# Optimization experiments

Measured on AMD Instinct MI355X. Metric: run time of the kernel, lower is better.

Reference implementation:

```python
import jax, jax.numpy as jnp
import numpy as np

MAXHD, MAXV, MINA, MAXA, DT = 100.0, 40.0, -6.0, 4.0, 0.1
NVEH, NT, IN_DIM, UNITS = 4096, 1024, 12, 20


def setup_inputs() -> dict:
    key = jax.random.key(0)
    ks = jax.random.split(key, 12)
    leadfol_inputs = jax.random.normal(ks[0], (NVEH, NT, IN_DIM), dtype=jnp.float32)
    init_state = jax.random.normal(ks[1], (NVEH, 2), dtype=jnp.float32)
    hidden_states = jnp.zeros((2, NVEH, UNITS), dtype=jnp.float32)
    s = 0.1
    return {
        "leadfol_inputs": leadfol_inputs,
        "init_state": init_state,
        "hidden_states": hidden_states,
        "kernel": s * jax.random.normal(ks[2], (IN_DIM, 4 * UNITS), dtype=jnp.float32),
        "rkernel": s * jax.random.normal(ks[3], (UNITS, 4 * UNITS), dtype=jnp.float32),
        "bias": jnp.zeros((4 * UNITS,), dtype=jnp.float32),
        "W2": s * jax.random.normal(ks[4], (UNITS, 10), dtype=jnp.float32),
        "b2": jnp.zeros((10,), dtype=jnp.float32),
        "Wlc": s * jax.random.normal(ks[5], (10, 3), dtype=jnp.float32),
        "blc": jnp.zeros((3,), dtype=jnp.float32),
        "W1": s * jax.random.normal(ks[6], (10, 1), dtype=jnp.float32),
        "b1": jnp.zeros((1,), dtype=jnp.float32),
    }


def reference(leadfol_inputs, init_state, hidden_states, kernel, rkernel, bias,
              W2, b2, Wlc, blc, W1, b1):
    # time-major for scan: (nt, nveh, 12)
    xs = jnp.transpose(leadfol_inputs, (1, 0, 2))
    pos0, spd0 = init_state[:, 0], init_state[:, 1]
    h0, c0 = hidden_states[0], hidden_states[1]

    def step(carry, x_t):
        pos, spd, h, c = carry
        lead_hd = (x_t[:, :3] - pos[:, None]) / MAXHD
        fol_hd = (pos[:, None] - x_t[:, 3:6]) / MAXHD
        spds = x_t[:, 6:] / MAXV
        inp = jnp.concatenate([lead_hd, fol_hd, spds], axis=1)  # (nveh, 12)
        inp = jnp.where(jnp.isnan(inp), jnp.ones_like(inp), inp)
        # Keras LSTMCell (inference, no dropout): gate order i, f, g, o
        z = inp @ kernel + h @ rkernel + bias
        i_g, f_g, g_g, o_g = jnp.split(z, 4, axis=1)
        c_new = jax.nn.sigmoid(f_g) * c + jax.nn.sigmoid(i_g) * jnp.tanh(g_g)
        h_new = jax.nn.sigmoid(o_g) * jnp.tanh(c_new)
        x2 = jax.nn.relu(h_new @ W2 + b2)          # (nveh, 10)
        lc = x2 @ Wlc + blc                          # (nveh, 3)
        acc_raw = (x2 @ W1 + b1)[:, 0]               # (nveh,)
        acc = (MAXA - MINA) * acc_raw + MINA
        pos_new = pos + DT * spd
        spd_new = spd + DT * acc
        return (pos_new, spd_new, h_new, c_new), (pos_new, lc)

    (pos_f, spd_f, h_f, c_f), (traj, lc_all) = jax.lax.scan(step, (pos0, spd0, h0, c0), xs)
    pred_traj = jnp.transpose(traj, (1, 0))            # (nveh, nt)
    pred_lc_action = jnp.transpose(lc_all, (1, 0, 2))  # (nveh, nt, 3)
    return pred_traj, pred_lc_action, spd_f, (h_f, c_f)
```

## Files before the change

kernel.cpp:

```cpp
#include <hip/hip_runtime.h>
#include <cstdint>

#define NVEH  4096
#define NT    1024
#define INW   12
#define UNITS 20

typedef float f32x2 __attribute__((ext_vector_type(2)));

#define PIN(v)  asm volatile("" : "+v"(v))

#define PKFMA_LO(acc, w, s2) \
    asm("v_pk_fma_f32 %0, %1, %2, %0 op_sel:[0,0,0] op_sel_hi:[1,0,1]" \
        : "+v"(acc) : "v"(w), "v"(s2))
#define PKFMA_HI(acc, w, s2) \
    asm("v_pk_fma_f32 %0, %1, %2, %0 op_sel:[0,1,0] op_sel_hi:[1,1,1]" \
        : "+v"(acc) : "v"(w), "v"(s2))
#define PKMUL_LO(dst, w, s2) \
    asm("v_pk_mul_f32 %0, %1, %2 op_sel:[0,0] op_sel_hi:[1,0]" \
        : "=v"(dst) : "v"(w), "v"(s2))
#define PKMUL_HI(dst, w, s2) \
    asm("v_pk_mul_f32 %0, %1, %2 op_sel:[0,1] op_sel_hi:[1,1]" \
        : "=v"(dst) : "v"(w), "v"(s2))

__device__ __forceinline__ float fexp2(float x) { return __builtin_amdgcn_exp2f(x); }
__device__ __forceinline__ float frcp(float x)  { return __builtin_amdgcn_rcpf(x); }

__device__ __forceinline__ void gload_lds16(const float* g, float* l) {
    __builtin_amdgcn_global_load_lds(
        (const __attribute__((address_space(1))) unsigned int*)g,
        (__attribute__((address_space(3))) unsigned int*)l,
        16, 0, 0);
}

__global__ __attribute__((amdgpu_waves_per_eu(2, 2))) __launch_bounds__(64)
void rnncf_kernel(const float* __restrict__ x,
                  const float* __restrict__ init_state,
                  const float* __restrict__ hs,
                  const float* __restrict__ K,
                  const float* __restrict__ R,
                  const float* __restrict__ bias,
                  const float* __restrict__ W2,
                  const float* __restrict__ b2,
                  const float* __restrict__ Wlc,
                  const float* __restrict__ blc,
                  const float* __restrict__ W1,
                  const float* __restrict__ b1,
                  float* __restrict__ out)
{
    const int lane = threadIdx.x;
    const int grp  = lane / 20;
    const int sub  = lane % 20;
    const int veh  = blockIdx.x * 3 + grp;
    const bool active = (grp < 3) && (veh < NVEH);
    const int vs = active ? veh : 0;

    __shared__ __align__(16) float x_lds[8][4][12];
    __shared__ __align__(16) float h_lds[4][20];
    __shared__ __align__(16) float x2_lds[4][12];

    const float s01l = -1.4426950408889634f;
    const float s01h = -1.4426950408889634f;
    const float s23l =  2.8853900817779268f;
    const float s23h = -1.4426950408889634f;
    f32x2 K01[12], K23[12], R01[20], R23[20], bz01, bz23;
    bz01[0] = s01l * bias[sub];      bz01[1] = s01h * bias[20 + sub];
    bz23[0] = s23l * bias[40 + sub]; bz23[1] = s23h * bias[60 + sub];
#pragma unroll
    for (int k = 0; k < 12; ++k) {
        K01[k][0] = s01l * K[k * 80 + sub];      K01[k][1] = s01h * K[k * 80 + 20 + sub];
        K23[k][0] = s23l * K[k * 80 + 40 + sub]; K23[k][1] = s23h * K[k * 80 + 60 + sub];
    }
#pragma unroll
    for (int k = 0; k < 20; ++k) {
        R01[k][0] = s01l * R[k * 80 + sub];      R01[k][1] = s01h * R[k * 80 + 20 + sub];
        R23[k][0] = s23l * R[k * 80 + 40 + sub]; R23[k][1] = s23h * R[k * 80 + 60 + sub];
    }
    const int mh = (sub < 10) ? sub : 9;
    f32x2 W2p[10];
#pragma unroll
    for (int u = 0; u < 10; ++u) {
        W2p[u][0] = W2[(2 * u) * 10 + mh];
        W2p[u][1] = W2[(2 * u + 1) * 10 + mh];
    }
    float b2s = b2[mh];
    const int jl = (sub < 3) ? sub : 0;
    f32x2 Wlcp[5];
#pragma unroll
    for (int m = 0; m < 5; ++m) {
        Wlcp[m][0] = Wlc[(2 * m) * 3 + jl];
        Wlcp[m][1] = Wlc[(2 * m + 1) * 3 + jl];
    }
    float blcs = blc[jl];
    PIN(bz01); PIN(bz23);
#pragma unroll
    for (int k = 0; k < 12; ++k) { PIN(K01[k]); PIN(K23[k]); }
#pragma unroll
    for (int k = 0; k < 20; ++k) { PIN(R01[k]); PIN(R23[k]); }
#pragma unroll
    for (int u = 0; u < 10; ++u) PIN(W2p[u]);
#pragma unroll
    for (int m = 0; m < 5; ++m) PIN(Wlcp[m]);
    PIN(b2s); PIN(blcs);

    float pos = init_state[vs * 2 + 0];
    float spd = init_state[vs * 2 + 1];
    float c   = hs[(size_t)NVEH * UNITS + (size_t)vs * UNITS + sub];
    float hnew = hs[(size_t)vs * UNITS + sub];

    h_lds[grp][sub] = hnew;
    __builtin_amdgcn_wave_barrier();
    f32x2 hrp[10];
#pragma unroll
    for (int q = 0; q < 5; ++q) {
        float4 v = ((const float4*)&h_lds[grp][0])[q];
        hrp[2*q][0]   = v.x; hrp[2*q][1]   = v.y;
        hrp[2*q+1][0] = v.z; hrp[2*q+1][1] = v.w;
    }
    __builtin_amdgcn_wave_barrier();

    const bool stg = (lane < 9);
    int sveh = blockIdx.x * 3 + lane / 3;
    if (sveh > NVEH - 1) sveh = NVEH - 1;
    const float* sgp = x + (size_t)sveh * NT * INW + (lane % 3) * 4;

    if (stg) {
#pragma unroll
        for (int t0 = 0; t0 < 8; ++t0)
            gload_lds16(sgp + (size_t)t0 * INW, &x_lds[t0][0][0]);
    }

    float* trajp = out + (size_t)vs * NT;
    float* lcp   = out + (size_t)NVEH * NT + (size_t)vs * NT * 3;

    for (int tb = 0; tb < NT; tb += 4) {
        asm volatile("s_waitcnt vmcnt(4)" ::: "memory");

#pragma unroll
        for (int j = 0; j < 4; ++j) {
            const int t = tb + j;

            float4 u0 = ((const float4*)&x_lds[t & 7][grp][0])[0];
            float4 u1 = ((const float4*)&x_lds[t & 7][grp][0])[1];
            float4 u2 = ((const float4*)&x_lds[t & 7][grp][0])[2];
            f32x2 x2p[5];
            if (t > 0) {
#pragma unroll
                for (int q = 0; q < 5; ++q)
                    x2p[q] = ((const f32x2*)&x2_lds[grp][0])[q];
            }

            const float pp = pos * 0.01f;
            f32x2 inp2[6];
            inp2[0][0] = fmaf(u0.x,  0.01f, -pp); inp2[0][1] = fmaf(u0.y,  0.01f, -pp);
            inp2[1][0] = fmaf(u0.z,  0.01f, -pp); inp2[1][1] = fmaf(u0.w, -0.01f,  pp);
            inp2[2][0] = fmaf(u1.x, -0.01f,  pp); inp2[2][1] = fmaf(u1.y, -0.01f,  pp);
            inp2[3][0] = u1.z * 0.025f;           inp2[3][1] = u1.w * 0.025f;
            inp2[4][0] = u2.x * 0.025f;           inp2[4][1] = u2.y * 0.025f;
            inp2[5][0] = u2.z * 0.025f;           inp2[5][1] = u2.w * 0.025f;

            f32x2 zK01 = bz01, zK23 = bz23;
#pragma unroll
            for (int q = 0; q < 6; ++q) {
                PKFMA_LO(zK01, K01[2*q],   inp2[q]);
                PKFMA_LO(zK23, K23[2*q],   inp2[q]);
                PKFMA_HI(zK01, K01[2*q+1], inp2[q]);
                PKFMA_HI(zK23, K23[2*q+1], inp2[q]);
            }
            f32x2 cE01, cO01, cE23, cO23;
            f32x2 dE01, dO01, dE23, dO23;
            PKMUL_LO(cE01, R01[0], hrp[0]);
            PKMUL_HI(cO01, R01[1], hrp[0]);
            PKMUL_LO(cE23, R23[0], hrp[0]);
            PKMUL_HI(cO23, R23[1], hrp[0]);
            PKMUL_LO(dE01, R01[10], hrp[5]);
            PKMUL_HI(dO01, R01[11], hrp[5]);
            PKMUL_LO(dE23, R23[10], hrp[5]);
            PKMUL_HI(dO23, R23[11], hrp[5]);
#pragma unroll
            for (int q = 1; q < 5; ++q) {
                PKFMA_LO(cE01, R01[2*q],   hrp[q]);
                PKFMA_HI(cO01, R01[2*q+1], hrp[q]);
                PKFMA_LO(cE23, R23[2*q],   hrp[q]);
                PKFMA_HI(cO23, R23[2*q+1], hrp[q]);
                PKFMA_LO(dE01, R01[2*q+10], hrp[q+5]);
                PKFMA_HI(dO01, R01[2*q+11], hrp[q+5]);
                PKFMA_LO(dE23, R23[2*q+10], hrp[q+5]);
                PKFMA_HI(dO23, R23[2*q+11], hrp[q+5]);
            }
            f32x2 z01 = (zK01 + (cE01 + cO01)) + (dE01 + dO01);
            f32x2 z23 = (zK23 + (cE23 + cO23)) + (dE23 + dO23);

            if (t > 0) {
                float a0 = b1[0], a1 = 0.0f;
#pragma unroll
                for (int m = 0; m < 5; ++m) {
                    a0 = fmaf(x2p[m][0], W1[2*m],   a0);
                    a1 = fmaf(x2p[m][1], W1[2*m+1], a1);
                }
                float accr = a0 + a1;
                spd = fmaf(0.1f, fmaf(10.0f, accr, -6.0f), spd);
                if (active && sub < 3) {
                    f32x2 lc2; lc2[0] = blcs; lc2[1] = 0.0f;
#pragma unroll
                    for (int m = 0; m < 5; ++m) {
                        asm("v_pk_fma_f32 %0, %1, %2, %0"
                            : "+v"(lc2) : "v"(x2p[m]), "v"(Wlcp[m]));
                    }
                    lcp[(t - 1) * 3 + sub] = lc2[0] + lc2[1];
                }
            }

            float ig = frcp(1.0f + fexp2(z01[0]));
            float fg = frcp(1.0f + fexp2(z01[1]));
            float gg = 1.0f - 2.0f * frcp(fexp2(z23[0]) + 1.0f);
            float og = frcp(1.0f + fexp2(z23[1]));
            c = fmaf(fg, c, ig * gg);
            float th = 1.0f - 2.0f * frcp(fexp2(2.8853900817779268f * c) + 1.0f);
            hnew = og * th;

            float posn = fmaf(0.1f, spd, pos);
            if (active && sub == 0) trajp[t] = posn;
            pos = posn;

            h_lds[grp][sub] = hnew;
#pragma unroll
            for (int q = 0; q < 5; ++q) {
                float4 v = ((const float4*)&h_lds[grp][0])[q];
                hrp[2*q][0]   = v.x; hrp[2*q][1]   = v.y;
                hrp[2*q+1][0] = v.z; hrp[2*q+1][1] = v.w;
            }

            f32x2 xm2; xm2[0] = b2s; xm2[1] = 0.0f;
#pragma unroll
            for (int u = 0; u < 10; ++u) {
                asm("v_pk_fma_f32 %0, %1, %2, %0"
                    : "+v"(xm2) : "v"(hrp[u]), "v"(W2p[u]));
            }
            float xm = fmaxf(xm2[0] + xm2[1], 0.0f);
            if (sub < 10) x2_lds[grp][sub] = xm;
        }

        if (stg) {
#pragma unroll
            for (int j = 0; j < 4; ++j) {
                int tt = tb + 8 + j; if (tt > NT - 1) tt = NT - 1;
                gload_lds16(sgp + (size_t)tt * INW, &x_lds[(tb + j) & 7][0][0]);
            }
        }
    }

    {
        f32x2 x2p[5];
#pragma unroll
        for (int q = 0; q < 5; ++q)
            x2p[q] = ((const f32x2*)&x2_lds[grp][0])[q];
        float a0 = b1[0], a1 = 0.0f;
#pragma unroll
        for (int m = 0; m < 5; ++m) {
            a0 = fmaf(x2p[m][0], W1[2*m],   a0);
            a1 = fmaf(x2p[m][1], W1[2*m+1], a1);
        }
        float accr = a0 + a1;
        spd = fmaf(0.1f, fmaf(10.0f, accr, -6.0f), spd);
        if (active && sub < 3) {
            f32x2 lc2; lc2[0] = blcs; lc2[1] = 0.0f;
#pragma unroll
            for (int m = 0; m < 5; ++m) {
                asm("v_pk_fma_f32 %0, %1, %2, %0"
                    : "+v"(lc2) : "v"(x2p[m]), "v"(Wlcp[m]));
            }
            lcp[(NT - 1) * 3 + sub] = lc2[0] + lc2[1];
        }
    }

    if (active) {
        float* spdf = out + (size_t)NVEH * NT * 4;
        float* hf   = spdf + NVEH;
        float* cf   = hf + (size_t)NVEH * UNITS;
        if (sub == 0) spdf[veh] = spd;
        hf[(size_t)veh * UNITS + sub] = hnew;
        cf[(size_t)veh * UNITS + sub] = c;
    }
}

extern "C" void kernel_launch(void* const* d_in, const int* in_sizes, int n_in,
                              void* d_out, int out_size, void* d_ws, size_t ws_size,
                              hipStream_t stream) {
    const float* x    = (const float*)d_in[0];
    const float* st0  = (const float*)d_in[1];
    const float* hs   = (const float*)d_in[2];
    const float* K    = (const float*)d_in[3];
    const float* R    = (const float*)d_in[4];
    const float* bias = (const float*)d_in[5];
    const float* W2   = (const float*)d_in[6];
    const float* b2   = (const float*)d_in[7];
    const float* Wlc  = (const float*)d_in[8];
    const float* blc  = (const float*)d_in[9];
    const float* W1   = (const float*)d_in[10];
    const float* b1   = (const float*)d_in[11];
    float* out = (float*)d_out;

    dim3 grid((NVEH + 2) / 3);
    dim3 block(64);
    hipLaunchKernelGGL(rnncf_kernel, grid, block, 0, stream,
                       x, st0, hs, K, R, bias, W2, b2, Wlc, blc, W1, b1, out);
}
```

Baseline: 716.0 us.

## Split each vehicle's gate matmul across three lane groups with shuffle reduction

Each wavefront now handles one vehicle instead of three, and the 32-input gate reduction is split across three 20-lane parts whose partial sums are combined with cross-lane shuffles. The position-dependent input term is factored out as a precomputed weight-sum times pos, so the next step's gate partials can be computed ahead of the position update. Per-lane register weights drop, which allows four waves per EU instead of two. In exchange the grid triples, each step adds shuffles, and lanes 60-63 do masked redundant work.

After: 1.168 ms. 1.63x slower.

```diff
diff --git a/kernel.cpp b/kernel.cpp
--- a/kernel.cpp
+++ b/kernel.cpp
@@ -16,15 +16,18 @@
 #define PKFMA_HI(acc, w, s2) \
     asm("v_pk_fma_f32 %0, %1, %2, %0 op_sel:[0,1,0] op_sel_hi:[1,1,1]" \
         : "+v"(acc) : "v"(w), "v"(s2))
-#define PKMUL_LO(dst, w, s2) \
-    asm("v_pk_mul_f32 %0, %1, %2 op_sel:[0,0] op_sel_hi:[1,0]" \
-        : "=v"(dst) : "v"(w), "v"(s2))
-#define PKMUL_HI(dst, w, s2) \
-    asm("v_pk_mul_f32 %0, %1, %2 op_sel:[0,1] op_sel_hi:[1,1]" \
-        : "=v"(dst) : "v"(w), "v"(s2))
+#define PKFMA(acc, a, b) \
+    asm("v_pk_fma_f32 %0, %1, %2, %0" : "+v"(acc) : "v"(a), "v"(b))
 
 __device__ __forceinline__ float fexp2(float x) { return __builtin_amdgcn_exp2f(x); }
 __device__ __forceinline__ float frcp(float x)  { return __builtin_amdgcn_rcpf(x); }
+
+__device__ __forceinline__ f32x2 shfl2(f32x2 v, int src) {
+    f32x2 r;
+    r[0] = __shfl(v[0], src, 64);
+    r[1] = __shfl(v[1], src, 64);
+    return r;
+}
 
 __device__ __forceinline__ void gload_lds16(const float* g, float* l) {
     __builtin_amdgcn_global_load_lds(
@@ -33,7 +36,7 @@
         16, 0, 0);
 }
 
-__global__ __attribute__((amdgpu_waves_per_eu(2, 2))) __launch_bounds__(64)
+__global__ __attribute__((amdgpu_waves_per_eu(4, 4))) __launch_bounds__(64)
 void rnncf_kernel(const float* __restrict__ x,
                   const float* __restrict__ init_state,
                   const float* __restrict__ hs,
@@ -49,147 +52,131 @@
                   float* __restrict__ out)
 {
     const int lane = threadIdx.x;
-    const int grp  = lane / 20;
-    const int sub  = lane % 20;
-    const int veh  = blockIdx.x * 3 + grp;
-    const bool active = (grp < 3) && (veh < NVEH);
-    const int vs = active ? veh : 0;
-
-    __shared__ __align__(16) float x_lds[8][4][12];
-    __shared__ __align__(16) float h_lds[4][20];
-    __shared__ __align__(16) float x2_lds[4][12];
-
-    const float s01l = -1.4426950408889634f;
-    const float s01h = -1.4426950408889634f;
-    const float s23l =  2.8853900817779268f;
-    const float s23h = -1.4426950408889634f;
-    f32x2 K01[12], K23[12], R01[20], R23[20], bz01, bz23;
-    bz01[0] = s01l * bias[sub];      bz01[1] = s01h * bias[20 + sub];
-    bz23[0] = s23l * bias[40 + sub]; bz23[1] = s23h * bias[60 + sub];
-#pragma unroll
-    for (int k = 0; k < 12; ++k) {
-        K01[k][0] = s01l * K[k * 80 + sub];      K01[k][1] = s01h * K[k * 80 + 20 + sub];
-        K23[k][0] = s23l * K[k * 80 + 40 + sub]; K23[k][1] = s23h * K[k * 80 + 60 + sub];
-    }
-#pragma unroll
-    for (int k = 0; k < 20; ++k) {
-        R01[k][0] = s01l * R[k * 80 + sub];      R01[k][1] = s01h * R[k * 80 + 20 + sub];
-        R23[k][0] = s23l * R[k * 80 + 40 + sub]; R23[k][1] = s23h * R[k * 80 + 60 + sub];
-    }
-    const int mh = (sub < 10) ? sub : 9;
-    f32x2 W2p[10];
-#pragma unroll
-    for (int u = 0; u < 10; ++u) {
-        W2p[u][0] = W2[(2 * u) * 10 + mh];
-        W2p[u][1] = W2[(2 * u + 1) * 10 + mh];
-    }
-    float b2s = b2[mh];
-    const int jl = (sub < 3) ? sub : 0;
-    f32x2 Wlcp[5];
-#pragma unroll
-    for (int m = 0; m < 5; ++m) {
-        Wlcp[m][0] = Wlc[(2 * m) * 3 + jl];
-        Wlcp[m][1] = Wlc[(2 * m + 1) * 3 + jl];
-    }
-    float blcs = blc[jl];
-    PIN(bz01); PIN(bz23);
-#pragma unroll
-    for (int k = 0; k < 12; ++k) { PIN(K01[k]); PIN(K23[k]); }
-#pragma unroll
-    for (int k = 0; k < 20; ++k) { PIN(R01[k]); PIN(R23[k]); }
-#pragma unroll
-    for (int u = 0; u < 10; ++u) PIN(W2p[u]);
-#pragma unroll
-    for (int m = 0; m < 5; ++m) PIN(Wlcp[m]);
-    PIN(b2s); PIN(blcs);
-
-    float pos = init_state[vs * 2 + 0];
-    float spd = init_state[vs * 2 + 1];
-    float c   = hs[(size_t)NVEH * UNITS + (size_t)vs * UNITS + sub];
-    float hnew = hs[(size_t)vs * UNITS + sub];
-
-    h_lds[grp][sub] = hnew;
+    const bool realp = (lane < 60);
+    const int part = realp ? (lane / 20) : 2;
+    const int u    = lane % 20;
+    const int veh  = blockIdx.x;
+
+    __shared__ __align__(16) float xf[8][12];
+    __shared__ __align__(16) float hb[20];
+    __shared__ __align__(16) float x2b[12];
+    __shared__ __align__(16) float wlcl[3][12];
+
+    const int hbase = (part == 0) ? 0 : (part == 1) ? 4 : 8;
+    const int xbase = part * 2;
+
+    const float L2E = 1.4426950408889634f;
+    const float sI = -L2E, sF = -L2E, sG = 2.0f * L2E, sO = -L2E;
+    f32x2 We01[6], Wo01[6], We23[6], Wo23[6], W2s[4];
+#pragma unroll
+    for (int j = 0; j < 4; ++j) {
+        const bool ok = realp && !(part == 2 && j >= 2);
+        const int hp = ok ? (hbase + j) : 0;
+        const int r0 = (2 * hp) * 80, r1 = (2 * hp + 1) * 80;
+        const float m = ok ? 1.0f : 0.0f;
+        We01[j][0] = m * sI * R[r0 + u];      We01[j][1] = m * sF * R[r0 + 20 + u];
+        Wo01[j][0] = m * sI * R[r1 + u];      Wo01[j][1] = m * sF * R[r1 + 20 + u];
+        We23[j][0] = m * sG * R[r0 + 40 + u]; We23[j][1] = m * sO * R[r0 + 60 + u];
+        Wo23[j][0] = m * sG * R[r1 + 40 + u]; Wo23[j][1] = m * sO * R[r1 + 60 + u];
+        const int mh_ = (u < 10) ? u : 9;
+        W2s[j][0] = m * W2[(2 * hp) * 10 + mh_];
+        W2s[j][1] = m * W2[(2 * hp + 1) * 10 + mh_];
+    }
+#pragma unroll
+    for (int j = 4; j < 6; ++j) {
+        const int xp = xbase + (j - 4);
+        const int k0 = 2 * xp, k1 = k0 + 1;
+        const float c0 = (k0 < 3) ? 0.01f : (k0 < 6) ? -0.01f : 0.025f;
+        const float c1 = (k1 < 3) ? 0.01f : (k1 < 6) ? -0.01f : 0.025f;
+        const float m = realp ? 1.0f : 0.0f;
+        We01[j][0] = m * sI * c0 * K[k0 * 80 + u];      We01[j][1] = m * sF * c0 * K[k0 * 80 + 20 + u];
+        Wo01[j][0] = m * sI * c1 * K[k1 * 80 + u];      Wo01[j][1] = m * sF * c1 * K[k1 * 80 + 20 + u];
+        We23[j][0] = m * sG * c0 * K[k0 * 80 + 40 + u]; We23[j][1] = m * sO * c0 * K[k0 * 80 + 60 + u];
+        Wo23[j][0] = m * sG * c1 * K[k1 * 80 + 40 + u]; Wo23[j][1] = m * sO * c1 * K[k1 * 80 + 60 + u];
+    }
+    f32x2 bzL01, bzL23, kd01, kd23;
+    bzL01[0]=bzL01[1]=bzL23[0]=bzL23[1]=0.0f;
+    kd01[0]=kd01[1]=kd23[0]=kd23[1]=0.0f;
+    if (lane < 20) {
+        bzL01[0] = sI * bias[u];      bzL01[1] = sF * bias[20 + u];
+        bzL23[0] = sG * bias[40 + u]; bzL23[1] = sO * bias[60 + u];
+        float aI = 0, aF = 0, aG = 0, aO = 0;
+        for (int k = 0; k < 6; ++k) {
+            float sgn = (k < 3) ? -0.01f : 0.01f;
+            aI += sgn * K[k * 80 + u];
+            aF += sgn * K[k * 80 + 20 + u];
+            aG += sgn * K[k * 80 + 40 + u];
+            aO += sgn * K[k * 80 + 60 + u];
+        }
+        kd01[0] = sI * aI; kd01[1] = sF * aF;
+        kd23[0] = sG * aG; kd23[1] = sO * aO;
+    }
+    const int mh = (u < 10) ? u : 9;
+    const float b2L  = (lane < 20) ? b2[mh] : 0.0f;
+    const float blcs = blc[(u < 3) ? u : 0];
+#pragma unroll
+    for (int j = 0; j < 6; ++j) { PIN(We01[j]); PIN(Wo01[j]); PIN(We23[j]); PIN(Wo23[j]); }
+#pragma unroll
+    for (int j = 0; j < 4; ++j) PIN(W2s[j]);
+    PIN(bzL01); PIN(bzL23); PIN(kd01); PIN(kd23);
+
+    for (int idx = lane; idx < 36; idx += 64) {
+        int j = idx / 12, m = idx % 12;
+        wlcl[j][m] = (m < 10) ? Wlc[m * 3 + j] : 0.0f;
+    }
+
+    float pos  = init_state[veh * 2 + 0];
+    float spd  = init_state[veh * 2 + 1];
+    float c    = hs[(size_t)NVEH * UNITS + (size_t)veh * UNITS + u];
+    float hnew = hs[(size_t)veh * UNITS + u];
+    if (lane < 20) hb[u] = hnew;
     __builtin_amdgcn_wave_barrier();
-    f32x2 hrp[10];
-#pragma unroll
-    for (int q = 0; q < 5; ++q) {
-        float4 v = ((const float4*)&h_lds[grp][0])[q];
-        hrp[2*q][0]   = v.x; hrp[2*q][1]   = v.y;
-        hrp[2*q+1][0] = v.z; hrp[2*q+1][1] = v.w;
-    }
-    __builtin_amdgcn_wave_barrier();
-
-    const bool stg = (lane < 9);
-    int sveh = blockIdx.x * 3 + lane / 3;
-    if (sveh > NVEH - 1) sveh = NVEH - 1;
-    const float* sgp = x + (size_t)sveh * NT * INW + (lane % 3) * 4;
-
-    if (stg) {
+
+    const bool stgL = (lane < 3);
+    const float* sgp = x + (size_t)veh * NT * INW + lane * 4;
+    if (stgL) {
 #pragma unroll
         for (int t0 = 0; t0 < 8; ++t0)
-            gload_lds16(sgp + (size_t)t0 * INW, &x_lds[t0][0][0]);
-    }
-
-    float* trajp = out + (size_t)vs * NT;
-    float* lcp   = out + (size_t)NVEH * NT + (size_t)vs * NT * 3;
+            gload_lds16(sgp + (size_t)t0 * INW, &xf[t0][0]);
+    }
+
+    const float* ha0p = &hb[(part == 0) ? 0 : (part == 1) ? 8 : 16];
+    const float* ha1p = &hb[(part == 0) ? 4 : (part == 1) ? 12 : 0];
+    const int xo = part * 4;
+    const int sA = (lane + 20) & 63, sB = (lane + 40) & 63;
+
+    float* trajp = out + (size_t)veh * NT;
+    float* lcp   = out + (size_t)NVEH * NT + (size_t)veh * NT * 3;
+
+    asm volatile("s_waitcnt vmcnt(7)" ::: "memory");
+    f32x2 zn01, zn23, op[6];
+    {
+        float4 r0 = *(const float4*)ha0p;
+        float4 r1 = *(const float4*)ha1p;
+        float4 r2 = *(const float4*)&xf[0][xo];
+        op[0][0]=r0.x; op[0][1]=r0.y; op[1][0]=r0.z; op[1][1]=r0.w;
+        op[2][0]=r1.x; op[2][1]=r1.y; op[3][0]=r1.z; op[3][1]=r1.w;
+        op[4][0]=r2.x; op[4][1]=r2.y; op[5][0]=r2.z; op[5][1]=r2.w;
+        zn01 = bzL01; zn23 = bzL23;
+#pragma unroll
+        for (int j = 0; j < 6; ++j) {
+            PKFMA_LO(zn01, We01[j], op[j]);
+            PKFMA_LO(zn23, We23[j], op[j]);
+            PKFMA_HI(zn01, Wo01[j], op[j]);
+            PKFMA_HI(zn23, Wo23[j], op[j]);
+        }
+    }
+    f32x2 x2p[5];
+#pragma unroll
+    for (int q = 0; q < 5; ++q) { x2p[q][0] = 0.0f; x2p[q][1] = 0.0f; }
+    f32x2 posp;
 
     for (int tb = 0; tb < NT; tb += 4) {
-        asm volatile("s_waitcnt vmcnt(4)" ::: "memory");
-
-#pragma unroll
-        for (int j = 0; j < 4; ++j) {
-            const int t = tb + j;
-
-            float4 u0 = ((const float4*)&x_lds[t & 7][grp][0])[0];
-            float4 u1 = ((const float4*)&x_lds[t & 7][grp][0])[1];
-            float4 u2 = ((const float4*)&x_lds[t & 7][grp][0])[2];
-            f32x2 x2p[5];
-            if (t > 0) {
-#pragma unroll
-                for (int q = 0; q < 5; ++q)
-                    x2p[q] = ((const f32x2*)&x2_lds[grp][0])[q];
-            }
-
-            const float pp = pos * 0.01f;
-            f32x2 inp2[6];
-            inp2[0][0] = fmaf(u0.x,  0.01f, -pp); inp2[0][1] = fmaf(u0.y,  0.01f, -pp);
-            inp2[1][0] = fmaf(u0.z,  0.01f, -pp); inp2[1][1] = fmaf(u0.w, -0.01f,  pp);
-            inp2[2][0] = fmaf(u1.x, -0.01f,  pp); inp2[2][1] = fmaf(u1.y, -0.01f,  pp);
-            inp2[3][0] = u1.z * 0.025f;           inp2[3][1] = u1.w * 0.025f;
-            inp2[4][0] = u2.x * 0.025f;           inp2[4][1] = u2.y * 0.025f;
-            inp2[5][0] = u2.z * 0.025f;           inp2[5][1] = u2.w * 0.025f;
-
-            f32x2 zK01 = bz01, zK23 = bz23;
-#pragma unroll
-            for (int q = 0; q < 6; ++q) {
-                PKFMA_LO(zK01, K01[2*q],   inp2[q]);
-                PKFMA_LO(zK23, K23[2*q],   inp2[q]);
-                PKFMA_HI(zK01, K01[2*q+1], inp2[q]);
-                PKFMA_HI(zK23, K23[2*q+1], inp2[q]);
-            }
-            f32x2 cE01, cO01, cE23, cO23;
-            f32x2 dE01, dO01, dE23, dO23;
-            PKMUL_LO(cE01, R01[0], hrp[0]);
-            PKMUL_HI(cO01, R01[1], hrp[0]);
-            PKMUL_LO(cE23, R23[0], hrp[0]);
-            PKMUL_HI(cO23, R23[1], hrp[0]);
-            PKMUL_LO(dE01, R01[10], hrp[5]);
-            PKMUL_HI(dO01, R01[11], hrp[5]);
-            PKMUL_LO(dE23, R23[10], hrp[5]);
-            PKMUL_HI(dO23, R23[11], hrp[5]);
-#pragma unroll
-            for (int q = 1; q < 5; ++q) {
-                PKFMA_LO(cE01, R01[2*q],   hrp[q]);
-                PKFMA_HI(cO01, R01[2*q+1], hrp[q]);
-                PKFMA_LO(cE23, R23[2*q],   hrp[q]);
-                PKFMA_HI(cO23, R23[2*q+1], hrp[q]);
-                PKFMA_LO(dE01, R01[2*q+10], hrp[q+5]);
-                PKFMA_HI(dO01, R01[2*q+11], hrp[q+5]);
-                PKFMA_LO(dE23, R23[2*q+10], hrp[q+5]);
-                PKFMA_HI(dO23, R23[2*q+11], hrp[q+5]);
-            }
-            f32x2 z01 = (zK01 + (cE01 + cO01)) + (dE01 + dO01);
-            f32x2 z23 = (zK23 + (cE23 + cO23)) + (dE23 + dO23);
+        asm volatile("s_waitcnt vmcnt(3)" ::: "memory");
+
+#pragma unroll
+        for (int j4 = 0; j4 < 4; ++j4) {
+            const int t = tb + j4;
 
             if (t > 0) {
                 float a0 = b1[0], a1 = 0.0f;
@@ -198,18 +185,31 @@
                     a0 = fmaf(x2p[m][0], W1[2*m],   a0);
                     a1 = fmaf(x2p[m][1], W1[2*m+1], a1);
                 }
-                float accr = a0 + a1;
-                spd = fmaf(0.1f, fmaf(10.0f, accr, -6.0f), spd);
-                if (active && sub < 3) {
+                spd = fmaf(0.1f, fmaf(10.0f, a0 + a1, -6.0f), spd);
+                if (lane < 3) {
+                    float4 wa = *(const float4*)&wlcl[lane][0];
+                    float4 wb = *(const float4*)&wlcl[lane][4];
+                    float2 wc = *(const float2*)&wlcl[lane][8];
+                    f32x2 w0, w1_, w2_, w3, w4;
+                    w0[0]=wa.x; w0[1]=wa.y; w1_[0]=wa.z; w1_[1]=wa.w;
+                    w2_[0]=wb.x; w2_[1]=wb.y; w3[0]=wb.z; w3[1]=wb.w;
+                    w4[0]=wc.x; w4[1]=wc.y;
                     f32x2 lc2; lc2[0] = blcs; lc2[1] = 0.0f;
-#pragma unroll
-                    for (int m = 0; m < 5; ++m) {
-                        asm("v_pk_fma_f32 %0, %1, %2, %0"
-                            : "+v"(lc2) : "v"(x2p[m]), "v"(Wlcp[m]));
-                    }
-                    lcp[(t - 1) * 3 + sub] = lc2[0] + lc2[1];
+                    PKFMA(lc2, x2p[0], w0); PKFMA(lc2, x2p[1], w1_);
+                    PKFMA(lc2, x2p[2], w2_); PKFMA(lc2, x2p[3], w3);
+                    PKFMA(lc2, x2p[4], w4);
+                    lcp[(t - 1) * 3 + lane] = lc2[0] + lc2[1];
                 }
             }
+            const float pold = pos;
+            pos = fmaf(0.1f, spd, pold);
+            if (lane == 0) trajp[t] = pos;
+            posp[0] = pold; posp[1] = pold;
+
+            f32x2 z01 = (zn01 + shfl2(zn01, sA)) + shfl2(zn01, sB);
+            f32x2 z23 = (zn23 + shfl2(zn23, sA)) + shfl2(zn23, sB);
+            PKFMA(z01, kd01, posp);
+            PKFMA(z23, kd23, posp);
 
             float ig = frcp(1.0f + fexp2(z01[0]));
             float fg = frcp(1.0f + fexp2(z01[1]));
@@ -219,68 +219,84 @@
             float th = 1.0f - 2.0f * frcp(fexp2(2.8853900817779268f * c) + 1.0f);
             hnew = og * th;
 
-            float posn = fmaf(0.1f, spd, pos);
-            if (active && sub == 0) trajp[t] = posn;
-            pos = posn;
-
-            h_lds[grp][sub] = hnew;
-#pragma unroll
-            for (int q = 0; q < 5; ++q) {
-                float4 v = ((const float4*)&h_lds[grp][0])[q];
-                hrp[2*q][0]   = v.x; hrp[2*q][1]   = v.y;
-                hrp[2*q+1][0] = v.z; hrp[2*q+1][1] = v.w;
-            }
-
-            f32x2 xm2; xm2[0] = b2s; xm2[1] = 0.0f;
-#pragma unroll
-            for (int u = 0; u < 10; ++u) {
-                asm("v_pk_fma_f32 %0, %1, %2, %0"
-                    : "+v"(xm2) : "v"(hrp[u]), "v"(W2p[u]));
-            }
-            float xm = fmaxf(xm2[0] + xm2[1], 0.0f);
-            if (sub < 10) x2_lds[grp][sub] = xm;
-        }
-
-        if (stg) {
+            if (lane < 20) hb[u] = hnew;
+            {
+                const int sl = (t + 1) & 7;
+                float4 r0 = *(const float4*)ha0p;
+                float4 r1 = *(const float4*)ha1p;
+                float4 r2 = *(const float4*)&xf[sl][xo];
+                op[0][0]=r0.x; op[0][1]=r0.y; op[1][0]=r0.z; op[1][1]=r0.w;
+                op[2][0]=r1.x; op[2][1]=r1.y; op[3][0]=r1.z; op[3][1]=r1.w;
+                op[4][0]=r2.x; op[4][1]=r2.y; op[5][0]=r2.z; op[5][1]=r2.w;
+            }
+
+            f32x2 xm2; xm2[0] = b2L; xm2[1] = 0.0f;
+            PKFMA(xm2, op[0], W2s[0]); PKFMA(xm2, op[1], W2s[1]);
+            PKFMA(xm2, op[2], W2s[2]); PKFMA(xm2, op[3], W2s[3]);
+            xm2 = (xm2 + shfl2(xm2, sA)) + shfl2(xm2, sB);
+            float xmv = fmaxf(xm2[0] + xm2[1], 0.0f);
+            if (lane < 10) x2b[lane] = xmv;
+            {
+                float4 a = *(const float4*)&x2b[0];
+                float4 b4 = *(const float4*)&x2b[4];
+                float2 e = *(const float2*)&x2b[8];
+                x2p[0][0]=a.x;  x2p[0][1]=a.y;  x2p[1][0]=a.z;  x2p[1][1]=a.w;
+                x2p[2][0]=b4.x; x2p[2][1]=b4.y; x2p[3][0]=b4.z; x2p[3][1]=b4.w;
+                x2p[4][0]=e.x;  x2p[4][1]=e.y;
+            }
+
+            zn01 = bzL01; zn23 = bzL23;
+#pragma unroll
+            for (int j = 0; j < 6; ++j) {
+                PKFMA_LO(zn01, We01[j], op[j]);
+                PKFMA_LO(zn23, We23[j], op[j]);
+                PKFMA_HI(zn01, Wo01[j], op[j]);
+                PKFMA_HI(zn23, Wo23[j], op[j]);
+            }
+        }
+
+        if (stgL) {
 #pragma unroll
             for (int j = 0; j < 4; ++j) {
                 int tt = tb + 8 + j; if (tt > NT - 1) tt = NT - 1;
-                gload_lds16(sgp + (size_t)tt * INW, &x_lds[(tb + j) & 7][0][0]);
+                gload_lds16(sgp + (size_t)tt * INW, &xf[(tb + j) & 7][0]);
             }
         }
     }
 
     {
-        f32x2 x2p[5];
-#pragma unroll
-        for (int q = 0; q < 5; ++q)
-            x2p[q] = ((const f32x2*)&x2_lds[grp][0])[q];
         float a0 = b1[0], a1 = 0.0f;
 #pragma unroll
         for (int m = 0; m < 5; ++m) {
             a0 = fmaf(x2p[m][0], W1[2*m],   a0);
             a1 = fmaf(x2p[m][1], W1[2*m+1], a1);
         }
-        float accr = a0 + a1;
-        spd = fmaf(0.1f, fmaf(10.0f, accr, -6.0f), spd);
-        if (active && sub < 3) {
+        spd = fmaf(0.1f, fmaf(10.0f, a0 + a1, -6.0f), spd);
+        if (lane < 3) {
+            float4 wa = *(const float4*)&wlcl[lane][0];
+            float4 wb = *(const float4*)&wlcl[lane][4];
+            float2 wc = *(const float2*)&wlcl[lane][8];
+            f32x2 w0, w1_, w2_, w3, w4;
+            w0[0]=wa.x; w0[1]=wa.y; w1_[0]=wa.z; w1_[1]=wa.w;
+            w2_[0]=wb.x; w2_[1]=wb.y; w3[0]=wb.z; w3[1]=wb.w;
+            w4[0]=wc.x; w4[1]=wc.y;
             f32x2 lc2; lc2[0] = blcs; lc2[1] = 0.0f;
-#pragma unroll
-            for (int m = 0; m < 5; ++m) {
-                asm("v_pk_fma_f32 %0, %1, %2, %0"
-                    : "+v"(lc2) : "v"(x2p[m]), "v"(Wlcp[m]));
-            }
-            lcp[(NT - 1) * 3 + sub] = lc2[0] + lc2[1];
-        }
-    }
-
-    if (active) {
+            PKFMA(lc2, x2p[0], w0); PKFMA(lc2, x2p[1], w1_);
+            PKFMA(lc2, x2p[2], w2_); PKFMA(lc2, x2p[3], w3);
+            PKFMA(lc2, x2p[4], w4);
+            lcp[(NT - 1) * 3 + lane] = lc2[0] + lc2[1];
+        }
+    }
+
+    {
         float* spdf = out + (size_t)NVEH * NT * 4;
         float* hf   = spdf + NVEH;
         float* cf   = hf + (size_t)NVEH * UNITS;
-        if (sub == 0) spdf[veh] = spd;
-        hf[(size_t)veh * UNITS + sub] = hnew;
-        cf[(size_t)veh * UNITS + sub] = c;
+        if (lane == 0) spdf[veh] = spd;
+        if (lane < 20) {
+            hf[(size_t)veh * UNITS + u] = hnew;
+            cf[(size_t)veh * UNITS + u] = c;
+        }
     }
 }
 
@@ -301,7 +317,7 @@
     const float* b1   = (const float*)d_in[11];
     float* out = (float*)d_out;
 
-    dim3 grid((NVEH + 2) / 3);
+    dim3 grid(NVEH);
     dim3 block(64);
     hipLaunchKernelGGL(rnncf_kernel, grid, block, 0, stream,
                        x, st0, hs, K, R, bias, W2, b2, Wlc, blc, W1, b1, out);
```
